# Optimization experiments

Measured on AMD Instinct MI355X. Metric: run time of the kernel, lower is better.

## Reference

```python
import jax, jax.numpy as jnp
import numpy as np

N_NODES = 100000
N_EDGES = 3200000
IN_CH = 16
HIDDEN = 32
NUM_HH = 1000


def setup_inputs() -> dict:
    key = jax.random.key(0)
    ks = jax.random.split(key, 10)
    x = jax.random.normal(ks[0], (N_NODES, IN_CH), dtype=jnp.float32)
    edge_index = jax.random.randint(ks[1], (2, N_EDGES), 0, N_NODES, dtype=jnp.int64)
    s = 1.0 / np.sqrt(IN_CH)
    w1_l = jax.random.uniform(ks[2], (IN_CH, HIDDEN), jnp.float32, -s, s)
    w1_r = jax.random.uniform(ks[3], (IN_CH, HIDDEN), jnp.float32, -s, s)
    b1 = jnp.zeros((HIDDEN,), jnp.float32)
    s2 = 1.0 / np.sqrt(HIDDEN)
    w2_l = jax.random.uniform(ks[4], (HIDDEN, HIDDEN), jnp.float32, -s2, s2)
    w2_r = jax.random.uniform(ks[5], (HIDDEN, HIDDEN), jnp.float32, -s2, s2)
    b2 = jnp.zeros((HIDDEN,), jnp.float32)
    fc_w = jax.random.uniform(ks[6], (HIDDEN, NUM_HH), jnp.float32, -s2, s2)
    fc_b = jnp.zeros((NUM_HH,), jnp.float32)
    return {"x": x, "edge_index": edge_index, "w1_l": w1_l, "w1_r": w1_r, "b1": b1,
            "w2_l": w2_l, "w2_r": w2_r, "b2": b2, "fc_w": fc_w, "fc_b": fc_b}


def _sage_conv(h, src, dst, w_l, w_r, b, n_nodes):
    # mean-aggregate source features onto targets (PyG SAGEConv, aggr='mean')
    msg = h[src]                                            # [E, F] gather
    agg = jax.ops.segment_sum(msg, dst, num_segments=n_nodes)
    cnt = jax.ops.segment_sum(jnp.ones((src.shape[0], 1), h.dtype), dst,
                              num_segments=n_nodes)
    mean = agg / jnp.maximum(cnt, 1.0)
    # out = lin_l(mean_neighbors) + lin_r(x); bias lives in lin_l
    return mean @ w_l + b + h @ w_r


def reference(x, edge_index, w1_l, w1_r, b1, w2_l, w2_r, b2, fc_w, fc_b):
    src, dst = edge_index[0], edge_index[1]
    n = x.shape[0]
    h = jax.nn.relu(_sage_conv(x, src, dst, w1_l, w1_r, b1, n))
    h = jax.nn.relu(_sage_conv(h, src, dst, w2_l, w2_r, b2, n))
    return h @ fc_w + fc_b
```

## Files before the change

### kernel.cpp

```cpp
#include <hip/hip_runtime.h>

#define N_NODES 100000
#define IN_CH 16
#define HIDDEN 32
#define NUM_HH 1000

#define NPB 128
#define NBUCK ((N_NODES + NPB - 1) / NPB)
#define NCHUNK 512
#define SCAN_N (NBUCK * NCHUNK)
#define S1_BLOCKS ((SCAN_N + 1023) / 1024)
#define SORT_CAP 6144

__global__ __launch_bounds__(256) void passA_count(const int* __restrict__ dst,
                                                   int* __restrict__ counts,
                                                   int n_edges, int cepb) {
  __shared__ int hist[NBUCK];
  for (int i = threadIdx.x; i < NBUCK; i += 256) hist[i] = 0;
  __syncthreads();
  const int s = blockIdx.x * cepb;
  const int e = min(n_edges, s + cepb);
  for (int i = s + threadIdx.x; i < e; i += 256)
    atomicAdd(&hist[dst[i] >> 7], 1);
  __syncthreads();
  for (int i = threadIdx.x; i < NBUCK; i += 256)
    counts[i * NCHUNK + blockIdx.x] = hist[i];
}

__global__ __launch_bounds__(1024) void scan_local(const int* __restrict__ in,
                                                   int* __restrict__ out,
                                                   int* __restrict__ partials) {
  __shared__ int tmp[1024];
  const int i = blockIdx.x * 1024 + threadIdx.x;
  const int v = (i < SCAN_N) ? in[i] : 0;
  tmp[threadIdx.x] = v;
  __syncthreads();
  for (int off = 1; off < 1024; off <<= 1) {
    int t = (threadIdx.x >= off) ? tmp[threadIdx.x - off] : 0;
    __syncthreads();
    tmp[threadIdx.x] += t;
    __syncthreads();
  }
  if (i < SCAN_N) out[i] = tmp[threadIdx.x] - v;
  if (threadIdx.x == 1023) partials[blockIdx.x] = tmp[threadIdx.x];
}

__global__ __launch_bounds__(512) void scan_partials(int* __restrict__ partials) {
  __shared__ int tmp[512];
  const int v = (threadIdx.x < S1_BLOCKS) ? partials[threadIdx.x] : 0;
  tmp[threadIdx.x] = v;
  __syncthreads();
  for (int off = 1; off < 512; off <<= 1) {
    int t = (threadIdx.x >= off) ? tmp[threadIdx.x - off] : 0;
    __syncthreads();
    tmp[threadIdx.x] += t;
    __syncthreads();
  }
  if (threadIdx.x < S1_BLOCKS) partials[threadIdx.x] = tmp[threadIdx.x] - v;
}

__global__ __launch_bounds__(1024) void scan_add(int* __restrict__ out,
                                                 const int* __restrict__ partials,
                                                 int* __restrict__ bucket_ptr,
                                                 int n_edges) {
  const int i = blockIdx.x * 1024 + threadIdx.x;
  if (i < SCAN_N) {
    const int v = out[i] + partials[blockIdx.x];
    out[i] = v;
    if ((i & (NCHUNK - 1)) == 0) bucket_ptr[i / NCHUNK] = v;
  }
  if (i == 0) bucket_ptr[NBUCK] = n_edges;
}

__global__ __launch_bounds__(256) void passB_scatter(
    const int* __restrict__ src, const int* __restrict__ dst,
    const int* __restrict__ offs, unsigned* __restrict__ packed, int n_edges,
    int cepb) {
  __shared__ int cur[NBUCK];
  for (int i = threadIdx.x; i < NBUCK; i += 256)
    cur[i] = offs[i * NCHUNK + blockIdx.x];
  __syncthreads();
  const int s = blockIdx.x * cepb;
  const int e = min(n_edges, s + cepb);
  for (int i = s + threadIdx.x; i < e; i += 256) {
    const int d = dst[i];
    const int b = d >> 7;
    const int pos = atomicAdd(&cur[b], 1);
    packed[pos] = (unsigned)src[i] | ((unsigned)(d & (NPB - 1)) << 17);
  }
}

__global__ __launch_bounds__(512) void bucket_sort(
    unsigned* __restrict__ packed, const int* __restrict__ bucket_ptr,
    int* __restrict__ row_ptr, int n_edges) {
  __shared__ unsigned stage[SORT_CAP];
  __shared__ int bins[NPB];
  __shared__ int scn[NPB];
  __shared__ int cur[NPB];
  const int b = blockIdx.x;
  const int s = bucket_ptr[b];
  const int cnt = bucket_ptr[b + 1] - s;
  const int tid = threadIdx.x;

  if (tid < NPB) bins[tid] = 0;
  __syncthreads();
  for (int i = tid; i < cnt; i += 512) {
    const unsigned pk = packed[s + i];
    stage[i] = pk;
    atomicAdd(&bins[pk >> 17], 1);
  }
  __syncthreads();
  if (tid < NPB) scn[tid] = bins[tid];
  __syncthreads();
  for (int off = 1; off < NPB; off <<= 1) {
    int t = (tid < NPB && tid >= off) ? scn[tid - off] : 0;
    __syncthreads();
    if (tid < NPB) scn[tid] += t;
    __syncthreads();
  }
  if (tid < NPB) {
    const int excl = scn[tid] - bins[tid];
    cur[tid] = excl;
    const int node = b * NPB + tid;
    if (node < N_NODES) row_ptr[node] = s + excl;
  }
  if (b == NBUCK - 1 && tid == 0) row_ptr[N_NODES] = n_edges;
  __syncthreads();
  for (int i = tid; i < cnt; i += 512) {
    const unsigned pk = stage[i];
    const int pos = atomicAdd(&cur[pk >> 17], 1);
    packed[s + pos] = pk & 0x1FFFFu;
  }
}

template <int CH>
__global__ __launch_bounds__(512) void sage_block(
    const float* __restrict__ feat, const int* __restrict__ row_ptr,
    const unsigned* __restrict__ adj, const int* __restrict__ bucket_ptr,
    const float* __restrict__ w_l, const float* __restrict__ w_r,
    const float* __restrict__ b, float* __restrict__ out) {
  constexpr int Q = CH / 4;
  constexpr int EPW = 64 / Q;
  __shared__ unsigned s_adj[SORT_CAP];
  __shared__ float wl[CH * HIDDEN];
  __shared__ float wr[CH * HIDDEN];
  __shared__ float bs[HIDDEN];
  __shared__ float mean_s[8][CH];
  __shared__ float xs[8][CH];

  const int tid = threadIdx.x;
  const int bk = blockIdx.x;
  const int base = bk * NPB;
  const int bstart = bucket_ptr[bk];
  const int bcnt = bucket_ptr[bk + 1] - bstart;

  for (int i = tid; i < CH * HIDDEN; i += 512) {
    wl[i] = w_l[i];
    wr[i] = w_r[i];
  }
  if (tid < HIDDEN) bs[tid] = b[tid];
  for (int i = tid; i < bcnt; i += 512) s_adj[i] = adj[bstart + i];
  __syncthreads();

  const int wave = tid >> 6;
  const int lane = tid & 63;
  const int q = lane & (Q - 1);
  const int esub = lane / Q;
  const int j = lane & 31;
  const int p = lane >> 5;

#pragma unroll 1
  for (int pass = 0; pass < NPB / 8; ++pass) {
    const int l = pass * 8 + wave;
    const int n = base + l;
    if (n < N_NODES) {
      const int s = row_ptr[n] - bstart;
      const int e = row_ptr[n + 1] - bstart;

      float4 xv = {0.f, 0.f, 0.f, 0.f};
      if (esub == 0) xv = ((const float4*)(feat + (size_t)n * CH))[q];

      float4 acc = {0.f, 0.f, 0.f, 0.f};
      for (int i = s + esub; i < e; i += EPW) {
        const int sn = (int)s_adj[i];
        const float4 v = ((const float4*)(feat + (size_t)sn * CH))[q];
        acc.x += v.x;
        acc.y += v.y;
        acc.z += v.z;
        acc.w += v.w;
      }
#pragma unroll
      for (int m = Q; m < 64; m <<= 1) {
        acc.x += __shfl_xor(acc.x, m, 64);
        acc.y += __shfl_xor(acc.y, m, 64);
        acc.z += __shfl_xor(acc.z, m, 64);
        acc.w += __shfl_xor(acc.w, m, 64);
      }
      const float inv = 1.0f / fmaxf((float)(e - s), 1.0f);
      if (esub == 0) {
        mean_s[wave][4 * q + 0] = acc.x * inv;
        mean_s[wave][4 * q + 1] = acc.y * inv;
        mean_s[wave][4 * q + 2] = acc.z * inv;
        mean_s[wave][4 * q + 3] = acc.w * inv;
        xs[wave][4 * q + 0] = xv.x;
        xs[wave][4 * q + 1] = xv.y;
        xs[wave][4 * q + 2] = xv.z;
        xs[wave][4 * q + 3] = xv.w;
      }
      __builtin_amdgcn_wave_barrier();

      float o = 0.f;
#pragma unroll
      for (int k = p * (CH / 2); k < (p + 1) * (CH / 2); ++k)
        o = fmaf(mean_s[wave][k], wl[k * HIDDEN + j],
                 fmaf(xs[wave][k], wr[k * HIDDEN + j], o));
      o += __shfl_xor(o, 32, 64);
      if (p == 0) out[(size_t)n * HIDDEN + j] = fmaxf(o + bs[j], 0.f);
      __builtin_amdgcn_wave_barrier();
    }
  }
}

#define FC_BN 128
__global__ __launch_bounds__(256) void fc_direct(
    const float* __restrict__ h, const float* __restrict__ fcw,
    const float* __restrict__ fcb, float* __restrict__ out) {
  const int tid = threadIdx.x;
  const int base = blockIdx.x * FC_BN;
  const int nvalid = min(FC_BN, N_NODES - base);

  float w[4][HIDDEN];
  float bias[4];
#pragma unroll
  for (int c = 0; c < 4; ++c) {
    const int j = c * 256 + tid;
    const bool valid = j < NUM_HH;
    bias[c] = valid ? fcb[j] : 0.f;
#pragma unroll
    for (int k = 0; k < HIDDEN; ++k)
      w[c][k] = valid ? fcw[k * NUM_HH + j] : 0.f;
  }

#pragma unroll 2
  for (int n = 0; n < nvalid; ++n) {
    const float4* hrow = (const float4*)(h + (size_t)(base + n) * HIDDEN);
    float a0 = bias[0], a1 = bias[1], a2 = bias[2], a3 = bias[3];
#pragma unroll
    for (int k4 = 0; k4 < HIDDEN / 4; ++k4) {
      const float4 hv = hrow[k4];
      a0 = fmaf(hv.x, w[0][4 * k4 + 0], a0);
      a0 = fmaf(hv.y, w[0][4 * k4 + 1], a0);
      a0 = fmaf(hv.z, w[0][4 * k4 + 2], a0);
      a0 = fmaf(hv.w, w[0][4 * k4 + 3], a0);
      a1 = fmaf(hv.x, w[1][4 * k4 + 0], a1);
      a1 = fmaf(hv.y, w[1][4 * k4 + 1], a1);
      a1 = fmaf(hv.z, w[1][4 * k4 + 2], a1);
      a1 = fmaf(hv.w, w[1][4 * k4 + 3], a1);
      a2 = fmaf(hv.x, w[2][4 * k4 + 0], a2);
      a2 = fmaf(hv.y, w[2][4 * k4 + 1], a2);
      a2 = fmaf(hv.z, w[2][4 * k4 + 2], a2);
      a2 = fmaf(hv.w, w[2][4 * k4 + 3], a2);
      a3 = fmaf(hv.x, w[3][4 * k4 + 0], a3);
      a3 = fmaf(hv.y, w[3][4 * k4 + 1], a3);
      a3 = fmaf(hv.z, w[3][4 * k4 + 2], a3);
      a3 = fmaf(hv.w, w[3][4 * k4 + 3], a3);
    }
    float* orow = out + (size_t)(base + n) * NUM_HH;
    orow[tid] = a0;
    orow[256 + tid] = a1;
    orow[512 + tid] = a2;
    if (768 + tid < NUM_HH) orow[768 + tid] = a3;
  }
}

extern "C" void kernel_launch(void* const* d_in, const int* in_sizes, int n_in,
                              void* d_out, int out_size, void* d_ws,
                              size_t ws_size, hipStream_t stream) {
  const float* x = (const float*)d_in[0];
  const int* edge = (const int*)d_in[1];
  const float* w1_l = (const float*)d_in[2];
  const float* w1_r = (const float*)d_in[3];
  const float* b1 = (const float*)d_in[4];
  const float* w2_l = (const float*)d_in[5];
  const float* w2_r = (const float*)d_in[6];
  const float* b2 = (const float*)d_in[7];
  const float* fc_w = (const float*)d_in[8];
  const float* fc_b = (const float*)d_in[9];
  float* out = (float*)d_out;

  const int n_edges = in_sizes[1] / 2;
  const int* src = edge;
  const int* dst = edge + n_edges;

  unsigned* packed = (unsigned*)d_ws;
  float* h1 = (float*)(packed + n_edges);
  float* h2 = h1 + (size_t)N_NODES * HIDDEN;
  int* counts = (int*)h2;
  int* offs = counts + SCAN_N;
  int* bucket_ptr = (int*)(h2 + (size_t)N_NODES * HIDDEN);
  int* partials = bucket_ptr + NBUCK + 1;
  int* row_ptr = partials + S1_BLOCKS + 1;

  const int cepb = (n_edges + NCHUNK - 1) / NCHUNK;
  const int fgrid = (N_NODES + FC_BN - 1) / FC_BN;

  passA_count<<<NCHUNK, 256, 0, stream>>>(dst, counts, n_edges, cepb);
  scan_local<<<S1_BLOCKS, 1024, 0, stream>>>(counts, offs, partials);
  scan_partials<<<1, 512, 0, stream>>>(partials);
  scan_add<<<S1_BLOCKS, 1024, 0, stream>>>(offs, partials, bucket_ptr, n_edges);
  passB_scatter<<<NCHUNK, 256, 0, stream>>>(src, dst, offs, packed, n_edges,
                                            cepb);
  bucket_sort<<<NBUCK, 512, 0, stream>>>(packed, bucket_ptr, row_ptr, n_edges);

  sage_block<IN_CH><<<NBUCK, 512, 0, stream>>>(x, row_ptr, packed, bucket_ptr,
                                               w1_l, w1_r, b1, h1);
  sage_block<HIDDEN><<<NBUCK, 512, 0, stream>>>(h1, row_ptr, packed, bucket_ptr,
                                                w2_l, w2_r, b2, h2);
  fc_direct<<<fgrid, 256, 0, stream>>>(h2, fc_w, fc_b, out);
}
```

Measured before the change: 424.0 us.

## Replace global prefix scan with fixed-capacity buckets and atomic slot reservation

```diff
diff --git a/kernel.cpp b/kernel.cpp
--- a/kernel.cpp
+++ b/kernel.cpp
@@ -8,104 +8,60 @@
 #define NPB 128
 #define NBUCK ((N_NODES + NPB - 1) / NPB)
 #define NCHUNK 512
-#define SCAN_N (NBUCK * NCHUNK)
-#define S1_BLOCKS ((SCAN_N + 1023) / 1024)
-#define SORT_CAP 6144
-
-__global__ __launch_bounds__(256) void passA_count(const int* __restrict__ dst,
-                                                   int* __restrict__ counts,
-                                                   int n_edges, int cepb) {
+#define CAP 4480
+
+__global__ __launch_bounds__(256) void passAB(
+    const int* __restrict__ src, const int* __restrict__ dst,
+    int* __restrict__ gcur, unsigned* __restrict__ packed, int n_edges,
+    int cepb) {
   __shared__ int hist[NBUCK];
-  for (int i = threadIdx.x; i < NBUCK; i += 256) hist[i] = 0;
-  __syncthreads();
+  __shared__ int rbase[NBUCK];
+  __shared__ int cur[NBUCK];
+  const int tid = threadIdx.x;
+  for (int i = tid; i < NBUCK; i += 256) {
+    hist[i] = 0;
+    cur[i] = 0;
+  }
+  __syncthreads();
+
   const int s = blockIdx.x * cepb;
   const int e = min(n_edges, s + cepb);
-  for (int i = s + threadIdx.x; i < e; i += 256)
-    atomicAdd(&hist[dst[i] >> 7], 1);
-  __syncthreads();
-  for (int i = threadIdx.x; i < NBUCK; i += 256)
-    counts[i * NCHUNK + blockIdx.x] = hist[i];
-}
-
-__global__ __launch_bounds__(1024) void scan_local(const int* __restrict__ in,
-                                                   int* __restrict__ out,
-                                                   int* __restrict__ partials) {
-  __shared__ int tmp[1024];
-  const int i = blockIdx.x * 1024 + threadIdx.x;
-  const int v = (i < SCAN_N) ? in[i] : 0;
-  tmp[threadIdx.x] = v;
-  __syncthreads();
-  for (int off = 1; off < 1024; off <<= 1) {
-    int t = (threadIdx.x >= off) ? tmp[threadIdx.x - off] : 0;
-    __syncthreads();
-    tmp[threadIdx.x] += t;
-    __syncthreads();
-  }
-  if (i < SCAN_N) out[i] = tmp[threadIdx.x] - v;
-  if (threadIdx.x == 1023) partials[blockIdx.x] = tmp[threadIdx.x];
-}
-
-__global__ __launch_bounds__(512) void scan_partials(int* __restrict__ partials) {
-  __shared__ int tmp[512];
-  const int v = (threadIdx.x < S1_BLOCKS) ? partials[threadIdx.x] : 0;
-  tmp[threadIdx.x] = v;
-  __syncthreads();
-  for (int off = 1; off < 512; off <<= 1) {
-    int t = (threadIdx.x >= off) ? tmp[threadIdx.x - off] : 0;
-    __syncthreads();
-    tmp[threadIdx.x] += t;
-    __syncthreads();
-  }
-  if (threadIdx.x < S1_BLOCKS) partials[threadIdx.x] = tmp[threadIdx.x] - v;
-}
-
-__global__ __launch_bounds__(1024) void scan_add(int* __restrict__ out,
-                                                 const int* __restrict__ partials,
-                                                 int* __restrict__ bucket_ptr,
-                                                 int n_edges) {
-  const int i = blockIdx.x * 1024 + threadIdx.x;
-  if (i < SCAN_N) {
-    const int v = out[i] + partials[blockIdx.x];
-    out[i] = v;
-    if ((i & (NCHUNK - 1)) == 0) bucket_ptr[i / NCHUNK] = v;
-  }
-  if (i == 0) bucket_ptr[NBUCK] = n_edges;
-}
-
-__global__ __launch_bounds__(256) void passB_scatter(
-    const int* __restrict__ src, const int* __restrict__ dst,
-    const int* __restrict__ offs, unsigned* __restrict__ packed, int n_edges,
-    int cepb) {
-  __shared__ int cur[NBUCK];
-  for (int i = threadIdx.x; i < NBUCK; i += 256)
-    cur[i] = offs[i * NCHUNK + blockIdx.x];
-  __syncthreads();
-  const int s = blockIdx.x * cepb;
-  const int e = min(n_edges, s + cepb);
-  for (int i = s + threadIdx.x; i < e; i += 256) {
+  for (int i = s + tid; i < e; i += 256) atomicAdd(&hist[dst[i] >> 7], 1);
+  __syncthreads();
+
+  for (int b = tid; b < NBUCK; b += 256) {
+    const int h = hist[b];
+    rbase[b] = h ? atomicAdd(&gcur[b], h) : 0;
+  }
+  __syncthreads();
+
+  for (int i = s + tid; i < e; i += 256) {
     const int d = dst[i];
     const int b = d >> 7;
-    const int pos = atomicAdd(&cur[b], 1);
-    packed[pos] = (unsigned)src[i] | ((unsigned)(d & (NPB - 1)) << 17);
+    const int off = atomicAdd(&cur[b], 1);
+    const int pos = rbase[b] + off;
+    if (pos < CAP)
+      packed[(size_t)b * CAP + pos] =
+          (unsigned)src[i] | ((unsigned)(d & (NPB - 1)) << 17);
   }
 }
 
 __global__ __launch_bounds__(512) void bucket_sort(
-    unsigned* __restrict__ packed, const int* __restrict__ bucket_ptr,
-    int* __restrict__ row_ptr, int n_edges) {
-  __shared__ unsigned stage[SORT_CAP];
+    unsigned* __restrict__ packed, const int* __restrict__ gcur,
+    int* __restrict__ row_ptr) {
+  __shared__ unsigned stage[CAP];
   __shared__ int bins[NPB];
   __shared__ int scn[NPB];
   __shared__ int cur[NPB];
   const int b = blockIdx.x;
-  const int s = bucket_ptr[b];
-  const int cnt = bucket_ptr[b + 1] - s;
+  const int base = b * CAP;
+  const int cnt = min(gcur[b], CAP);
   const int tid = threadIdx.x;
 
   if (tid < NPB) bins[tid] = 0;
   __syncthreads();
   for (int i = tid; i < cnt; i += 512) {
-    const unsigned pk = packed[s + i];
+    const unsigned pk = packed[base + i];
     stage[i] = pk;
     atomicAdd(&bins[pk >> 17], 1);
   }
@@ -122,26 +78,26 @@
     const int excl = scn[tid] - bins[tid];
     cur[tid] = excl;
     const int node = b * NPB + tid;
-    if (node < N_NODES) row_ptr[node] = s + excl;
-  }
-  if (b == NBUCK - 1 && tid == 0) row_ptr[N_NODES] = n_edges;
+    if (node < N_NODES) row_ptr[node] = base + excl;
+  }
+  if (b == NBUCK - 1 && tid == 0) row_ptr[N_NODES] = base + cnt;
   __syncthreads();
   for (int i = tid; i < cnt; i += 512) {
     const unsigned pk = stage[i];
     const int pos = atomicAdd(&cur[pk >> 17], 1);
-    packed[s + pos] = pk & 0x1FFFFu;
+    packed[base + pos] = pk & 0x1FFFFu;
   }
 }
 
 template <int CH>
 __global__ __launch_bounds__(512) void sage_block(
     const float* __restrict__ feat, const int* __restrict__ row_ptr,
-    const unsigned* __restrict__ adj, const int* __restrict__ bucket_ptr,
+    const unsigned* __restrict__ adj, const int* __restrict__ gcur,
     const float* __restrict__ w_l, const float* __restrict__ w_r,
     const float* __restrict__ b, float* __restrict__ out) {
   constexpr int Q = CH / 4;
   constexpr int EPW = 64 / Q;
-  __shared__ unsigned s_adj[SORT_CAP];
+  __shared__ unsigned s_adj[CAP];
   __shared__ float wl[CH * HIDDEN];
   __shared__ float wr[CH * HIDDEN];
   __shared__ float bs[HIDDEN];
@@ -151,8 +107,8 @@
   const int tid = threadIdx.x;
   const int bk = blockIdx.x;
   const int base = bk * NPB;
-  const int bstart = bucket_ptr[bk];
-  const int bcnt = bucket_ptr[bk + 1] - bstart;
+  const int bstart = bk * CAP;
+  const int bcnt = min(gcur[bk], CAP);
 
   for (int i = tid; i < CH * HIDDEN; i += 512) {
     wl[i] = w_l[i];
@@ -175,7 +131,7 @@
     const int n = base + l;
     if (n < N_NODES) {
       const int s = row_ptr[n] - bstart;
-      const int e = row_ptr[n + 1] - bstart;
+      const int e = (l == NPB - 1) ? bcnt : row_ptr[n + 1] - bstart;
 
       float4 xv = {0.f, 0.f, 0.f, 0.f};
       if (esub == 0) xv = ((const float4*)(feat + (size_t)n * CH))[q];
@@ -293,28 +249,21 @@
   const int* dst = edge + n_edges;
 
   unsigned* packed = (unsigned*)d_ws;
-  float* h1 = (float*)(packed + n_edges);
+  float* h1 = (float*)(packed + (size_t)NBUCK * CAP);
   float* h2 = h1 + (size_t)N_NODES * HIDDEN;
-  int* counts = (int*)h2;
-  int* offs = counts + SCAN_N;
-  int* bucket_ptr = (int*)(h2 + (size_t)N_NODES * HIDDEN);
-  int* partials = bucket_ptr + NBUCK + 1;
-  int* row_ptr = partials + S1_BLOCKS + 1;
+  int* gcur = (int*)(h2 + (size_t)N_NODES * HIDDEN);
+  int* row_ptr = gcur + NBUCK;
 
   const int cepb = (n_edges + NCHUNK - 1) / NCHUNK;
   const int fgrid = (N_NODES + FC_BN - 1) / FC_BN;
 
-  passA_count<<<NCHUNK, 256, 0, stream>>>(dst, counts, n_edges, cepb);
-  scan_local<<<S1_BLOCKS, 1024, 0, stream>>>(counts, offs, partials);
-  scan_partials<<<1, 512, 0, stream>>>(partials);
-  scan_add<<<S1_BLOCKS, 1024, 0, stream>>>(offs, partials, bucket_ptr, n_edges);
-  passB_scatter<<<NCHUNK, 256, 0, stream>>>(src, dst, offs, packed, n_edges,
-                                            cepb);
-  bucket_sort<<<NBUCK, 512, 0, stream>>>(packed, bucket_ptr, row_ptr, n_edges);
-
-  sage_block<IN_CH><<<NBUCK, 512, 0, stream>>>(x, row_ptr, packed, bucket_ptr,
-                                               w1_l, w1_r, b1, h1);
-  sage_block<HIDDEN><<<NBUCK, 512, 0, stream>>>(h1, row_ptr, packed, bucket_ptr,
+  hipMemsetAsync(gcur, 0, NBUCK * sizeof(int), stream);
+  passAB<<<NCHUNK, 256, 0, stream>>>(src, dst, gcur, packed, n_edges, cepb);
+  bucket_sort<<<NBUCK, 512, 0, stream>>>(packed, gcur, row_ptr);
+
+  sage_block<IN_CH><<<NBUCK, 512, 0, stream>>>(x, row_ptr, packed, gcur, w1_l,
+                                               w1_r, b1, h1);
+  sage_block<HIDDEN><<<NBUCK, 512, 0, stream>>>(h1, row_ptr, packed, gcur,
                                                 w2_l, w2_r, b2, h2);
   fc_direct<<<fgrid, 256, 0, stream>>>(h2, fc_w, fc_b, out);
 }
```

New measurement: 426.3 us. Within noise of the previous version (+0.5%).
